# Kernel optimization log

Hardware: AMD Instinct MI355X
Metric: run time of the kernel (lower is better)

Reference implementation:

```python
import jax, jax.numpy as jnp
import numpy as np
import math

C = 256
NUM_CLASSES = 80
NUM_CONVS = 4
GROUPS = 32
LEVEL_SHAPES = [(100, 152), (50, 76), (25, 38), (13, 19), (7, 10)]
BATCH = 2


def conv2d(x, w, b):
    # x: [N,C,H,W], w: [O,I,3,3] -> SAME padding, stride 1
    y = jax.lax.conv_general_dilated(x, w, window_strides=(1, 1), padding='SAME',
                                     dimension_numbers=('NCHW', 'OIHW', 'NCHW'))
    return y + b[None, :, None, None]


def group_norm(x, w, b, groups=GROUPS, eps=1e-5):
    N, Ch, H, W = x.shape
    xg = x.reshape(N, groups, Ch // groups, H, W)
    mu = jnp.mean(xg, axis=(2, 3, 4), keepdims=True)
    var = jnp.var(xg, axis=(2, 3, 4), keepdims=True)
    xg = (xg - mu) * jax.lax.rsqrt(var + eps)
    x = xg.reshape(N, Ch, H, W)
    return x * w[None, :, None, None] + b[None, :, None, None]


def tower(x, cw, cb, gw, gb):
    for i in range(NUM_CONVS):
        x = jax.nn.relu(group_norm(conv2d(x, cw[i], cb[i]), gw[i], gb[i]))
    return x


def flatten_head(y, c):
    # [N, A*c, H, W] -> [N, H*W*A, c]  (matches view/permute/reshape in torch)
    N, AC, H, W = y.shape
    A = AC // c
    return y.reshape(N, A, c, H, W).transpose(0, 3, 4, 1, 2).reshape(N, H * W * A, c)


def setup_inputs() -> dict:
    key = jax.random.key(0)
    ks = iter(jax.random.split(key, 64))
    inp = {}
    for i, (h, w) in enumerate(LEVEL_SHAPES):
        inp[f"feat{i}"] = jax.random.normal(next(ks), (BATCH, C, h, w), jnp.float32)
    def cw(shape):  # conv weights init std=0.01 as in torch module
        return jax.random.normal(next(ks), shape, jnp.float32) * 0.01
    inp["cls_conv_w"] = cw((NUM_CONVS, C, C, 3, 3))
    inp["cls_conv_b"] = jnp.zeros((NUM_CONVS, C), jnp.float32)
    inp["cls_gn_w"] = jnp.ones((NUM_CONVS, C), jnp.float32)
    inp["cls_gn_b"] = jnp.zeros((NUM_CONVS, C), jnp.float32)
    inp["cls_out_w"] = cw((NUM_CLASSES, C, 3, 3))
    inp["cls_out_b"] = jnp.full((NUM_CLASSES,), -math.log(99.0), jnp.float32)  # prior prob 0.01
    inp["reg_conv_w"] = cw((NUM_CONVS, C, C, 3, 3))
    inp["reg_conv_b"] = jnp.zeros((NUM_CONVS, C), jnp.float32)
    inp["reg_gn_w"] = jnp.ones((NUM_CONVS, C), jnp.float32)
    inp["reg_gn_b"] = jnp.zeros((NUM_CONVS, C), jnp.float32)
    for name, oc in [("bbox", 4), ("ctr", 1), ("dim", 3), ("ori", 1), ("kp", 16), ("depth", 1)]:
        inp[f"{name}_w"] = cw((oc, C, 3, 3))
        inp[f"{name}_b"] = jnp.zeros((oc,), jnp.float32)
    return inp


def reference(feat0, feat1, feat2, feat3, feat4,
              cls_conv_w, cls_conv_b, cls_gn_w, cls_gn_b, cls_out_w, cls_out_b,
              reg_conv_w, reg_conv_b, reg_gn_w, reg_gn_b,
              bbox_w, bbox_b, ctr_w, ctr_b, dim_w, dim_b,
              ori_w, ori_b, kp_w, kp_b, depth_w, depth_b):
    feats = [feat0, feat1, feat2, feat3, feat4]
    cls_all, bbox_all, ctr_all, dim_all, ori_all, kp_all, depth_all = ([] for _ in range(7))
    for f in feats:
        cf = tower(f, cls_conv_w, cls_conv_b, cls_gn_w, cls_gn_b)
        cls_all.append(flatten_head(conv2d(cf, cls_out_w, cls_out_b), NUM_CLASSES))
        rf = tower(f, reg_conv_w, reg_conv_b, reg_gn_w, reg_gn_b)
        bbox_all.append(flatten_head(jax.nn.relu(conv2d(rf, bbox_w, bbox_b)), 4))
        ctr_all.append(flatten_head(conv2d(rf, ctr_w, ctr_b), 1))
        dim_all.append(flatten_head(conv2d(rf, dim_w, dim_b), 3))
        ori_all.append(flatten_head(conv2d(rf, ori_w, ori_b), 1))
        kp_all.append(flatten_head(conv2d(rf, kp_w, kp_b), 16))
        depth_all.append(flatten_head(conv2d(rf, depth_w, depth_b), 1))
    cat = lambda xs: jnp.concatenate(xs, axis=1)
    return (cat(cls_all), cat(bbox_all), cat(ctr_all), cat(dim_all),
            cat(ori_all), cat(kp_all), cat(depth_all))
```

## Files before the change

### kernel.cpp

```cpp
#include <hip/hip_runtime.h>
#include <stdint.h>

typedef unsigned short ushort_t;
typedef __bf16 bf16x8 __attribute__((ext_vector_type(8)));
typedef float f32x4 __attribute__((ext_vector_type(4)));

#define TOTAL_HW 20267
#define PTOT 21267

__constant__ int d_RB[26] = {3242720,3242720,3242720,3242720, 3404856, 3445390,3445390,3445390,
                             3566992, 3607526,3607526,3607526,3607526,3607526,3607526,3607526,3607526,
                             3607526,3607526,3607526,3607526,3607526,3607526,3607526,3607526, 4256070};
__constant__ int d_RM[26] = {4,4,4,4, 1, 3,3,3, 1, 16,16,16,16,16,16,16,16,16,16,16,16,16,16,16,16, 1};
__constant__ int d_RC[26] = {0,1,2,3, 0, 0,1,2, 0, 0,1,2,3,4,5,6,7,8,9,10,11,12,13,14,15, 0};

__constant__ int F_TC[6]   = {0,238,298,314,318,320};
__constant__ int F_TL[5]   = {119,30,8,2,1};
__constant__ int F_W[5]    = {152,76,38,19,10};
__constant__ int F_HW[5]   = {15200,3800,950,247,70};
__constant__ int F_PB[5]   = {0,15708,19764,20844,21159};
__constant__ int F_LOFF[5] = {0,15200,19000,19950,20197};
__constant__ int F_PC[6]   = {0,508,764,894,962,1000};
__constant__ int F_H[5]    = {100,50,25,13,7};

__device__ __forceinline__ ushort_t f2bf(float f) {
    union { float f; uint32_t i; } x; x.f = f;
    uint32_t r = x.i + 0x7fffu + ((x.i >> 16) & 1u);
    return (ushort_t)(r >> 16);
}
__device__ __forceinline__ float bf2f(ushort_t u) {
    union { uint32_t i; float f; } x; x.i = ((uint32_t)u) << 16; return x.f;
}
__device__ __forceinline__ void gld16(const ushort_t* g, ushort_t* lds) {
    __builtin_amdgcn_global_load_lds((const __attribute__((address_space(1))) void*)g,
                                     (__attribute__((address_space(3))) void*)lds, 16, 0, 0);
}

__global__ __launch_bounds__(256) void wtrans_tower_k(const float* __restrict__ src,
                                                      ushort_t* __restrict__ dst)
{
    int id = blockIdx.x * 256 + threadIdx.x;
    int oc = id >> 8, ic = id & 255;
    const float* s = src + (size_t)(oc * 256 + ic) * 9;
    ushort_t* d = dst + oc * 256 + ic;
    #pragma unroll
    for (int t = 0; t < 9; t++) d[t * 65536] = f2bf(s[t]);
}
__global__ __launch_bounds__(256) void wtrans_cls_k(const float* __restrict__ src,
                                                    ushort_t* __restrict__ dst)
{
    int id = blockIdx.x * 256 + threadIdx.x;
    int oc = id >> 8, ic = id & 255;
    ushort_t* d = dst + oc * 256 + ic;
    if (oc < 80) {
        const float* s = src + (size_t)(oc * 256 + ic) * 9;
        #pragma unroll
        for (int t = 0; t < 9; t++) d[t * 32768] = f2bf(s[t]);
    } else {
        #pragma unroll
        for (int t = 0; t < 9; t++) d[t * 32768] = 0;
    }
}
__global__ __launch_bounds__(256) void wtrans_reg_k(
    const float* bbox_w, const float* ctr_w, const float* dim_w,
    const float* ori_w,  const float* kp_w,  const float* depth_w,
    const float* bbox_b, const float* ctr_b, const float* dim_b,
    const float* ori_b,  const float* kp_b,  const float* depth_b,
    ushort_t* __restrict__ dst, float* __restrict__ RegBias)
{
    int id = blockIdx.x * 256 + threadIdx.x;
    int oc = id >> 8, ic = id & 255;
    ushort_t* d = dst + oc * 256 + ic;
    if (oc < 26) {
        const float* s; int c;
        if (oc < 4)       { s = bbox_w;  c = oc; }
        else if (oc < 5)  { s = ctr_w;   c = 0; }
        else if (oc < 8)  { s = dim_w;   c = oc - 5; }
        else if (oc < 9)  { s = ori_w;   c = 0; }
        else if (oc < 25) { s = kp_w;    c = oc - 9; }
        else              { s = depth_w; c = 0; }
        const float* sp = s + (size_t)(c * 256 + ic) * 9;
        #pragma unroll
        for (int t = 0; t < 9; t++) d[t * 32768] = f2bf(sp[t]);
    } else {
        #pragma unroll
        for (int t = 0; t < 9; t++) d[t * 32768] = 0;
    }
    if (id < 26) {
        const float* b; int c;
        if (id < 4)       { b = bbox_b;  c = id; }
        else if (id < 5)  { b = ctr_b;   c = 0; }
        else if (id < 8)  { b = dim_b;   c = id - 5; }
        else if (id < 9)  { b = ori_b;   c = 0; }
        else if (id < 25) { b = kp_b;    c = id - 9; }
        else              { b = depth_b; c = 0; }
        RegBias[id] = b[c];
    }
}

__global__ __launch_bounds__(256) void pad_k(ushort_t* b0, ushort_t* b1, ushort_t* b2, ushort_t* b3)
{
    int u = blockIdx.x * 256 + threadIdx.x;
    if (u >= 256000) return;
    int chunk = u & 31; u >>= 5;
    int buf = u & 3; u >>= 2;
    int n = (u >= 1000) ? 1 : 0; int pidx = u - n * 1000;
    int l = 0;
    #pragma unroll
    for (int i = 1; i < 5; i++) if (pidx >= F_PC[i]) l = i;
    int q = pidx - F_PC[l];
    int W = F_W[l], H = F_H[l], Wp = W + 2;
    int py, px;
    if (q < Wp) { py = 0; px = q; }
    else if (q < 2 * Wp) { py = H + 1; px = q - Wp; }
    else { int q2 = q - 2 * Wp; py = 1 + (q2 >> 1); px = (q2 & 1) ? (Wp - 1) : 0; }
    ushort_t* base = b0;
    if (buf == 1) base = b1; else if (buf == 2) base = b2; else if (buf == 3) base = b3;
    *(uint4*)(base + ((size_t)n * PTOT + F_PB[l] + py * Wp + px) * 256 + chunk * 8) = uint4{0u,0u,0u,0u};
}

__global__ __launch_bounds__(256) void packF_k(
    const float* f0, const float* f1, const float* f2,
    const float* f3, const float* f4, ushort_t* __restrict__ S)
{
    __shared__ ushort_t tile[64][65];
    const int PCUM[6] = {0, 1904, 2384, 2504, 2536, 2552};
    const int PT[5]   = {238, 60, 15, 4, 2};
    int bid = blockIdx.x;
    int l = 0;
    #pragma unroll
    for (int i = 1; i < 5; i++) if (bid >= PCUM[i]) l = i;
    int r = bid - PCUM[l];
    int per_n = PT[l] * 4;
    int n = (r >= per_n) ? 1 : 0; r -= n * per_n;
    int pb = r >> 2, cb = r & 3;
    const float* fs = f0;
    if (l == 1) fs = f1; else if (l == 2) fs = f2; else if (l == 3) fs = f3; else if (l == 4) fs = f4;
    int HW = F_HW[l], W = F_W[l], Wp = W + 2;
    int p0 = pb * 64, c0 = cb * 64;
    int t = threadIdx.x;
    #pragma unroll
    for (int i = 0; i < 16; i++) {
        int idx = i * 256 + t; int cl = idx >> 6, pl = idx & 63;
        int p = p0 + pl; ushort_t v = 0;
        if (p < HW) v = f2bf(fs[(size_t)(n * 256 + c0 + cl) * HW + p]);
        tile[cl][pl] = v;
    }
    __syncthreads();
    ushort_t* ob = S + ((size_t)n * PTOT + F_PB[l]) * 256;
    #pragma unroll
    for (int i = 0; i < 16; i++) {
        int idx = i * 256 + t; int pl = idx >> 6, cl = idx & 63;
        int p = p0 + pl;
        if (p < HW) {
            int y = p / W, x = p - y * W;
            ob[((y + 1) * Wp + (x + 1)) * 256 + c0 + cl] = tile[cl][pl];
        }
    }
}

__global__ __launch_bounds__(256) void convT_k(
    const ushort_t* __restrict__ srcC, const ushort_t* __restrict__ srcR,
    ushort_t* __restrict__ dstC, ushort_t* __restrict__ dstR,
    const ushort_t* __restrict__ wtAll,
    const float* __restrict__ biasC, const float* __restrict__ biasR,
    float* __restrict__ stats, int L)
{
    __shared__ __align__(16) ushort_t As[2][4096];
    __shared__ __align__(16) ushort_t Bs[2][4096];

    int gid = blockIdx.x;
    int xcd = gid & 7, idx = gid >> 3;
    int bid = xcd * 40 + (idx >> 2);
    int oc0 = (idx & 1) * 128;
    int tw = (idx >> 1) & 1;

    const ushort_t* src = tw ? srcR : srcC;
    ushort_t* dst = tw ? dstR : dstC;
    const ushort_t* wt = wtAll + (size_t)(tw * 4 + L) * 589824;
    const float* bias = (tw ? biasR : biasC) + L * 256;

    int l = 0;
    #pragma unroll
    for (int i = 1; i < 5; i++) if (bid >= F_TC[i]) l = i;
    int r = bid - F_TC[l];
    int tl = F_TL[l];
    int n = (r >= tl) ? 1 : 0; int tile = r - n * tl;
    int W = F_W[l], HW = F_HW[l], Wp = W + 2;
    int px0 = tile * 128;
    const ushort_t* sbase = src + ((size_t)n * PTOT + F_PB[l]) * 256;
    ushort_t* obase = dst + ((size_t)n * PTOT + F_PB[l]) * 256;

    int tid = threadIdx.x, wv = tid >> 6, ln = tid & 63;
    int wr = wv >> 1, wc = wv & 1;

    int aoff[2], boff[2];
    #pragma unroll
    for (int j = 0; j < 2; j++) {
        int rloc = (wv * 2 + j) * 16 + (ln >> 2);
        int p = px0 + rloc; if (p > HW - 1) p = HW - 1;
        int y = p / W, x = p - y * W;
        int c = ((ln & 3) - (rloc >> 1)) & 3;
        aoff[j] = ((y + 1) * Wp + (x + 1)) * 256 + c * 8;
        boff[j] = (oc0 + rloc) * 256 + c * 8;
    }

    f32x4 acc[4][4];
    #pragma unroll
    for (int mi = 0; mi < 4; mi++)
        #pragma unroll
        for (int ni = 0; ni < 4; ni++) acc[mi][ni] = f32x4{0.f, 0.f, 0.f, 0.f};

    {
        int tapo = (-Wp - 1) * 256;
        #pragma unroll
        for (int j = 0; j < 2; j++) gld16(sbase + aoff[j] + tapo, &As[0][(wv * 2 + j) * 512]);
        #pragma unroll
        for (int j = 0; j < 2; j++) gld16(wt + boff[j], &Bs[0][(wv * 2 + j) * 512]);
    }

    #pragma unroll 2
    for (int it = 0; it < 72; ++it) {
        __syncthreads();
        int nx = it + 1;
        if (nx < 72) {
            int tp = nx >> 3, kc = (nx & 7) << 5;
            int ky = tp / 3, kx = tp - ky * 3;
            int tapo = ((ky - 1) * Wp + (kx - 1)) * 256 + kc;
            const ushort_t* wtap = wt + tp * 65536 + kc;
            int b = nx & 1;
            #pragma unroll
            for (int j = 0; j < 2; j++) gld16(sbase + aoff[j] + tapo, &As[b][(wv * 2 + j) * 512]);
            #pragma unroll
            for (int j = 0; j < 2; j++) gld16(wtap + boff[j], &Bs[b][(wv * 2 + j) * 512]);
        }
        int b = it & 1;
        bf16x8 af[4], bg[4];
        #pragma unroll
        for (int mi = 0; mi < 4; mi++) {
            int rA = wr * 64 + mi * 16 + (ln & 15);
            int ch = ((ln >> 4) + (rA >> 1)) & 3;
            af[mi] = *(const bf16x8*)&As[b][rA * 32 + ch * 8];
        }
        #pragma unroll
        for (int ni = 0; ni < 4; ni++) {
            int rB = wc * 64 + ni * 16 + (ln & 15);
            int ch = ((ln >> 4) + (rB >> 1)) & 3;
            bg[ni] = *(const bf16x8*)&Bs[b][rB * 32 + ch * 8];
        }
        #pragma unroll
        for (int mi = 0; mi < 4; mi++)
            #pragma unroll
            for (int ni = 0; ni < 4; ni++)
                acc[mi][ni] = __builtin_amdgcn_mfma_f32_16x16x32_bf16(af[mi], bg[ni], acc[mi][ni], 0, 0, 0);
    }

    #pragma unroll
    for (int ni = 0; ni < 4; ni++) {
        int oc = oc0 + wc * 64 + ni * 16 + (ln & 15);
        float bv = bias[oc];
        float s = 0.f, q = 0.f;
        #pragma unroll
        for (int mi = 0; mi < 4; mi++) {
            int pb = px0 + wr * 64 + mi * 16 + ((ln >> 4) << 2);
            if (pb < HW) {
                int y = pb / W, x = pb - y * W;
                #pragma unroll
                for (int rr2 = 0; rr2 < 4; rr2++) {
                    int p = pb + rr2;
                    if (p < HW) {
                        float v = acc[mi][ni][rr2] + bv;
                        obase[((y + 1) * Wp + (x + 1)) * 256 + oc] = f2bf(v);
                        s += v; q += v * v;
                    }
                    x++; if (x == W) { x = 0; y++; }
                }
            }
        }
        s += __shfl_xor(s, 16, 64); q += __shfl_xor(q, 16, 64);
        s += __shfl_xor(s, 32, 64); q += __shfl_xor(q, 32, 64);
        s += __shfl_xor(s, 1, 64);  q += __shfl_xor(q, 1, 64);
        s += __shfl_xor(s, 2, 64);  q += __shfl_xor(q, 2, 64);
        s += __shfl_xor(s, 4, 64);  q += __shfl_xor(q, 4, 64);
        if (ln == 0 || ln == 8) {
            int g = (oc0 + wc * 64 + ni * 16 + (ln & 8)) >> 3;
            float* st = stats + (size_t)((tw * 4 + L) * 5 + l) * 128 + (n * 32 + g) * 2;
            atomicAdd(st, s); atomicAdd(st + 1, q);
        }
    }
}

__global__ __launch_bounds__(256) void convH_k(
    const ushort_t* __restrict__ srcC, const ushort_t* __restrict__ srcR,
    const ushort_t* __restrict__ wtC, const ushort_t* __restrict__ wtR,
    const float* __restrict__ biasC, const float* __restrict__ biasR,
    float* __restrict__ outF)
{
    __shared__ __align__(16) ushort_t As[2][4096];
    __shared__ __align__(16) ushort_t Bs[2][4096];

    int gid = blockIdx.x;
    int xcd = gid & 7, idx = gid >> 3;
    int bid = xcd * 40 + (idx >> 1);
    int mode = idx & 1;

    const ushort_t* src = mode ? srcR : srcC;
    const ushort_t* wt  = mode ? wtR  : wtC;
    const float* bias   = mode ? biasR : biasC;

    int l = 0;
    #pragma unroll
    for (int i = 1; i < 5; i++) if (bid >= F_TC[i]) l = i;
    int r = bid - F_TC[l];
    int tl = F_TL[l];
    int n = (r >= tl) ? 1 : 0; int tile = r - n * tl;
    int W = F_W[l], HW = F_HW[l], Wp = W + 2;
    int px0 = tile * 128;
    const ushort_t* sbase = src + ((size_t)n * PTOT + F_PB[l]) * 256;

    int tid = threadIdx.x, wv = tid >> 6, ln = tid & 63;
    int wr = wv >> 1, wc = wv & 1;

    int aoff[2], boff[2];
    #pragma unroll
    for (int j = 0; j < 2; j++) {
        int rloc = (wv * 2 + j) * 16 + (ln >> 2);
        int p = px0 + rloc; if (p > HW - 1) p = HW - 1;
        int y = p / W, x = p - y * W;
        int c = ((ln & 3) - (rloc >> 1)) & 3;
        aoff[j] = ((y + 1) * Wp + (x + 1)) * 256 + c * 8;
        boff[j] = rloc * 256 + c * 8;
    }

    f32x4 acc[4][4];
    #pragma unroll
    for (int mi = 0; mi < 4; mi++)
        #pragma unroll
        for (int ni = 0; ni < 4; ni++) acc[mi][ni] = f32x4{0.f, 0.f, 0.f, 0.f};

    {
        int tapo = (-Wp - 1) * 256;
        #pragma unroll
        for (int j = 0; j < 2; j++) gld16(sbase + aoff[j] + tapo, &As[0][(wv * 2 + j) * 512]);
        #pragma unroll
        for (int j = 0; j < 2; j++) gld16(wt + boff[j], &Bs[0][(wv * 2 + j) * 512]);
    }

    #pragma unroll 2
    for (int it = 0; it < 72; ++it) {
        __syncthreads();
        int nx = it + 1;
        if (nx < 72) {
            int tp = nx >> 3, kc = (nx & 7) << 5;
            int ky = tp / 3, kx = tp - ky * 3;
            int tapo = ((ky - 1) * Wp + (kx - 1)) * 256 + kc;
            const ushort_t* wtap = wt + tp * 32768 + kc;
            int b = nx & 1;
            #pragma unroll
            for (int j = 0; j < 2; j++) gld16(sbase + aoff[j] + tapo, &As[b][(wv * 2 + j) * 512]);
            #pragma unroll
            for (int j = 0; j < 2; j++) gld16(wtap + boff[j], &Bs[b][(wv * 2 + j) * 512]);
        }
        int b = it & 1;
        bf16x8 af[4], bg[4];
        #pragma unroll
        for (int mi = 0; mi < 4; mi++) {
            int rA = wr * 64 + mi * 16 + (ln & 15);
            int ch = ((ln >> 4) + (rA >> 1)) & 3;
            af[mi] = *(const bf16x8*)&As[b][rA * 32 + ch * 8];
        }
        #pragma unroll
        for (int ni = 0; ni < 4; ni++) {
            int rB = wc * 64 + ni * 16 + (ln & 15);
            int ch = ((ln >> 4) + (rB >> 1)) & 3;
            bg[ni] = *(const bf16x8*)&Bs[b][rB * 32 + ch * 8];
        }
        #pragma unroll
        for (int mi = 0; mi < 4; mi++)
            #pragma unroll
            for (int ni = 0; ni < 4; ni++)
                acc[mi][ni] = __builtin_amdgcn_mfma_f32_16x16x32_bf16(af[mi], bg[ni], acc[mi][ni], 0, 0, 0);
    }

    #pragma unroll
    for (int ni = 0; ni < 4; ni++) {
        int oc = wc * 64 + ni * 16 + (ln & 15);
        bool valid = mode ? (oc < 26) : (oc < 80);
        if (valid) {
            float bv = bias[oc];
            int rb = 0, rm = 80, rc = oc; bool rl = false;
            if (mode) { rb = d_RB[oc]; rm = d_RM[oc]; rc = d_RC[oc]; rl = (oc < 4); }
            #pragma unroll
            for (int mi = 0; mi < 4; mi++) {
                int pb = px0 + wr * 64 + mi * 16 + ((ln >> 4) << 2);
                #pragma unroll
                for (int rr2 = 0; rr2 < 4; rr2++) {
                    int p = pb + rr2;
                    if (p < HW) {
                        float v = acc[mi][ni][rr2] + bv;
                        if (rl) v = fmaxf(v, 0.f);
                        int pg = n * TOTAL_HW + F_LOFF[l] + p;
                        outF[rb + (size_t)pg * rm + rc] = v;
                    }
                }
            }
        }
    }
}

__global__ __launch_bounds__(256) void normF_k(
    ushort_t* __restrict__ bufC, ushort_t* __restrict__ bufR,
    const float* __restrict__ stats,
    const float* __restrict__ gwC, const float* __restrict__ gwR,
    const float* __restrict__ gbC, const float* __restrict__ gbR, int L)
{
    int u = blockIdx.x * 256 + threadIdx.x;
    if (u >= 2594176) return;
    int tw = (u >= 1297088) ? 1 : 0; u -= tw * 1297088;
    int n = (u >= 648544) ? 1 : 0; u -= n * 648544;
    int cp = u >> 5, g = u & 31;
    int l = 0;
    #pragma unroll
    for (int i = 1; i < 5; i++) if (cp >= F_LOFF[i]) l = i;
    int p = cp - F_LOFF[l];
    int W = F_W[l], HW = F_HW[l];
    int y = p / W, x = p - y * W;
    const float* st = stats + (size_t)((tw * 4 + L) * 5 + l) * 128 + (n * 32 + g) * 2;
    float cnt = 8.0f * (float)HW;
    float mean = st[0] / cnt;
    float var = st[1] / cnt - mean * mean;
    float inv = rsqrtf(fmaxf(var, 0.f) + 1e-5f);
    const float* gw = (tw ? gwR : gwC) + L * 256 + g * 8;
    const float* gb = (tw ? gbR : gbC) + L * 256 + g * 8;
    ushort_t* buf = tw ? bufR : bufC;
    ushort_t* ptr = buf + (((size_t)n * PTOT + F_PB[l]) + (y + 1) * (W + 2) + (x + 1)) * 256 + g * 8;
    uint4 din = *(const uint4*)ptr;
    uint4 dout;
    const ushort_t* xi = (const ushort_t*)&din;
    ushort_t* oi = (ushort_t*)&dout;
    #pragma unroll
    for (int i = 0; i < 8; i++) {
        float v = (bf2f(xi[i]) - mean) * inv * gw[i] + gb[i];
        oi[i] = f2bf(fmaxf(v, 0.f));
    }
    *(uint4*)ptr = dout;
}


extern "C" void kernel_launch(void* const* d_in, const int* in_sizes, int n_in,
                              void* d_out, int out_size, void* d_ws, size_t ws_size,
                              hipStream_t stream) {
    const float* feats[5] = {(const float*)d_in[0], (const float*)d_in[1],
                             (const float*)d_in[2], (const float*)d_in[3],
                             (const float*)d_in[4]};
    const float* cls_conv_w = (const float*)d_in[5];
    const float* cls_conv_b = (const float*)d_in[6];
    const float* cls_gn_w   = (const float*)d_in[7];
    const float* cls_gn_b   = (const float*)d_in[8];
    const float* cls_out_w  = (const float*)d_in[9];
    const float* cls_out_b  = (const float*)d_in[10];
    const float* reg_conv_w = (const float*)d_in[11];
    const float* reg_conv_b = (const float*)d_in[12];
    const float* reg_gn_w   = (const float*)d_in[13];
    const float* reg_gn_b   = (const float*)d_in[14];

    char* wsb = (char*)d_ws;
    float* Stats     = (float*)wsb;
    float* RegBias   = (float*)(wsb + 20480);
    ushort_t* TowerWtAll = (ushort_t*)(wsb + 20608);
    ushort_t* WtCls  = (ushort_t*)(wsb + 9457792);
    ushort_t* WtReg  = (ushort_t*)(wsb + 10047616);
    ushort_t* S  = (ushort_t*)(wsb + 10637440);
    ushort_t* Ac = (ushort_t*)(wsb + 32414848);
    ushort_t* Ar = (ushort_t*)(wsb + 54192256);
    ushort_t* Br = (ushort_t*)(wsb + 75969664);
    float* outf  = (float*)d_out;

    hipMemsetAsync(d_ws, 0, 20608, stream);
    pad_k<<<1000, 256, 0, stream>>>(S, Ac, Ar, Br);

    for (int tw = 0; tw < 2; tw++) {
        const float* conv_w = tw ? reg_conv_w : cls_conv_w;
        for (int L = 0; L < 4; L++)
            wtrans_tower_k<<<256, 256, 0, stream>>>(conv_w + (size_t)L * 589824,
                                                    TowerWtAll + (size_t)(tw * 4 + L) * 589824);
    }
    wtrans_cls_k<<<128, 256, 0, stream>>>(cls_out_w, WtCls);
    wtrans_reg_k<<<128, 256, 0, stream>>>(
        (const float*)d_in[15], (const float*)d_in[17], (const float*)d_in[19],
        (const float*)d_in[21], (const float*)d_in[23], (const float*)d_in[25],
        (const float*)d_in[16], (const float*)d_in[18], (const float*)d_in[20],
        (const float*)d_in[22], (const float*)d_in[24], (const float*)d_in[26],
        WtReg, RegBias);

    packF_k<<<2552, 256, 0, stream>>>(feats[0], feats[1], feats[2], feats[3], feats[4], S);

    ushort_t* sc[4] = {S,  Ac, S,  Ac};
    ushort_t* dc[4] = {Ac, S,  Ac, S };
    ushort_t* sr[4] = {S,  Ar, Br, Ar};
    ushort_t* dr[4] = {Ar, Br, Ar, Br};
    for (int L = 0; L < 4; L++) {
        convT_k<<<1280, 256, 0, stream>>>(
            sc[L], sr[L], dc[L], dr[L], TowerWtAll, cls_conv_b, reg_conv_b, Stats, L);
        normF_k<<<10134, 256, 0, stream>>>(
            dc[L], dr[L], Stats, cls_gn_w, reg_gn_w, cls_gn_b, reg_gn_b, L);
    }
    convH_k<<<640, 256, 0, stream>>>(S, Br, WtCls, WtReg, cls_out_b, RegBias, outf);
}
```

Baseline: 919.4 us.

## Triple-buffer conv GEMM LDS tiles with partial vmcnt waits and MFMA priority

Moves the convT and convH implicit-GEMM main loops from double to triple LDS buffering, prefetching two K-steps ahead. The full __syncthreads is replaced by an inline s_waitcnt vmcnt(4) plus s_barrier, so only the older in-flight global-to-LDS loads must complete before each step. MFMA blocks are wrapped in s_setprio to favour matrix issue. LDS use per block grows from 32KB to 48KB, which may reduce occupancy, and the hand-written vmcnt counting depends on each step issuing exactly four loads per thread.

```diff
diff --git a/kernel.cpp b/kernel.cpp
--- a/kernel.cpp
+++ b/kernel.cpp
@@ -166,8 +166,8 @@
     const float* __restrict__ biasC, const float* __restrict__ biasR,
     float* __restrict__ stats, int L)
 {
-    __shared__ __align__(16) ushort_t As[2][4096];
-    __shared__ __align__(16) ushort_t Bs[2][4096];
+    __shared__ __align__(16) ushort_t As[3][4096];
+    __shared__ __align__(16) ushort_t Bs[3][4096];
 
     int gid = blockIdx.x;
     int xcd = gid & 7, idx = gid >> 3;
@@ -217,24 +217,33 @@
         for (int j = 0; j < 2; j++) gld16(sbase + aoff[j] + tapo, &As[0][(wv * 2 + j) * 512]);
         #pragma unroll
         for (int j = 0; j < 2; j++) gld16(wt + boff[j], &Bs[0][(wv * 2 + j) * 512]);
-    }
-
-    #pragma unroll 2
+        asm volatile("" ::: "memory");
+        #pragma unroll
+        for (int j = 0; j < 2; j++) gld16(sbase + aoff[j] + tapo + 32, &As[1][(wv * 2 + j) * 512]);
+        #pragma unroll
+        for (int j = 0; j < 2; j++) gld16(wt + 32 + boff[j], &Bs[1][(wv * 2 + j) * 512]);
+    }
+
+    #pragma unroll 3
     for (int it = 0; it < 72; ++it) {
-        __syncthreads();
-        int nx = it + 1;
+        if (it < 71) {
+            asm volatile("s_waitcnt vmcnt(4) lgkmcnt(0)\n\ts_barrier" ::: "memory");
+        } else {
+            asm volatile("s_waitcnt vmcnt(0) lgkmcnt(0)\n\ts_barrier" ::: "memory");
+        }
+        int nx = it + 2;
         if (nx < 72) {
             int tp = nx >> 3, kc = (nx & 7) << 5;
             int ky = tp / 3, kx = tp - ky * 3;
             int tapo = ((ky - 1) * Wp + (kx - 1)) * 256 + kc;
             const ushort_t* wtap = wt + tp * 65536 + kc;
-            int b = nx & 1;
-            #pragma unroll
-            for (int j = 0; j < 2; j++) gld16(sbase + aoff[j] + tapo, &As[b][(wv * 2 + j) * 512]);
-            #pragma unroll
-            for (int j = 0; j < 2; j++) gld16(wtap + boff[j], &Bs[b][(wv * 2 + j) * 512]);
-        }
-        int b = it & 1;
+            int bs = nx % 3;
+            #pragma unroll
+            for (int j = 0; j < 2; j++) gld16(sbase + aoff[j] + tapo, &As[bs][(wv * 2 + j) * 512]);
+            #pragma unroll
+            for (int j = 0; j < 2; j++) gld16(wtap + boff[j], &Bs[bs][(wv * 2 + j) * 512]);
+        }
+        int b = it % 3;
         bf16x8 af[4], bg[4];
         #pragma unroll
         for (int mi = 0; mi < 4; mi++) {
@@ -248,11 +257,13 @@
             int ch = ((ln >> 4) + (rB >> 1)) & 3;
             bg[ni] = *(const bf16x8*)&Bs[b][rB * 32 + ch * 8];
         }
+        __builtin_amdgcn_s_setprio(1);
         #pragma unroll
         for (int mi = 0; mi < 4; mi++)
             #pragma unroll
             for (int ni = 0; ni < 4; ni++)
                 acc[mi][ni] = __builtin_amdgcn_mfma_f32_16x16x32_bf16(af[mi], bg[ni], acc[mi][ni], 0, 0, 0);
+        __builtin_amdgcn_s_setprio(0);
     }
 
     #pragma unroll
@@ -296,8 +307,8 @@
     const float* __restrict__ biasC, const float* __restrict__ biasR,
     float* __restrict__ outF)
 {
-    __shared__ __align__(16) ushort_t As[2][4096];
-    __shared__ __align__(16) ushort_t Bs[2][4096];
+    __shared__ __align__(16) ushort_t As[3][4096];
+    __shared__ __align__(16) ushort_t Bs[3][4096];
 
     int gid = blockIdx.x;
     int xcd = gid & 7, idx = gid >> 3;
@@ -344,24 +355,33 @@
         for (int j = 0; j < 2; j++) gld16(sbase + aoff[j] + tapo, &As[0][(wv * 2 + j) * 512]);
         #pragma unroll
         for (int j = 0; j < 2; j++) gld16(wt + boff[j], &Bs[0][(wv * 2 + j) * 512]);
-    }
-
-    #pragma unroll 2
+        asm volatile("" ::: "memory");
+        #pragma unroll
+        for (int j = 0; j < 2; j++) gld16(sbase + aoff[j] + tapo + 32, &As[1][(wv * 2 + j) * 512]);
+        #pragma unroll
+        for (int j = 0; j < 2; j++) gld16(wt + 32 + boff[j], &Bs[1][(wv * 2 + j) * 512]);
+    }
+
+    #pragma unroll 3
     for (int it = 0; it < 72; ++it) {
-        __syncthreads();
-        int nx = it + 1;
+        if (it < 71) {
+            asm volatile("s_waitcnt vmcnt(4) lgkmcnt(0)\n\ts_barrier" ::: "memory");
+        } else {
+            asm volatile("s_waitcnt vmcnt(0) lgkmcnt(0)\n\ts_barrier" ::: "memory");
+        }
+        int nx = it + 2;
         if (nx < 72) {
             int tp = nx >> 3, kc = (nx & 7) << 5;
             int ky = tp / 3, kx = tp - ky * 3;
             int tapo = ((ky - 1) * Wp + (kx - 1)) * 256 + kc;
             const ushort_t* wtap = wt + tp * 32768 + kc;
-            int b = nx & 1;
-            #pragma unroll
-            for (int j = 0; j < 2; j++) gld16(sbase + aoff[j] + tapo, &As[b][(wv * 2 + j) * 512]);
-            #pragma unroll
-            for (int j = 0; j < 2; j++) gld16(wtap + boff[j], &Bs[b][(wv * 2 + j) * 512]);
-        }
-        int b = it & 1;
+            int bs = nx % 3;
+            #pragma unroll
+            for (int j = 0; j < 2; j++) gld16(sbase + aoff[j] + tapo, &As[bs][(wv * 2 + j) * 512]);
+            #pragma unroll
+            for (int j = 0; j < 2; j++) gld16(wtap + boff[j], &Bs[bs][(wv * 2 + j) * 512]);
+        }
+        int b = it % 3;
         bf16x8 af[4], bg[4];
         #pragma unroll
         for (int mi = 0; mi < 4; mi++) {
@@ -375,11 +395,13 @@
             int ch = ((ln >> 4) + (rB >> 1)) & 3;
             bg[ni] = *(const bf16x8*)&Bs[b][rB * 32 + ch * 8];
         }
+        __builtin_amdgcn_s_setprio(1);
         #pragma unroll
         for (int mi = 0; mi < 4; mi++)
             #pragma unroll
             for (int ni = 0; ni < 4; ni++)
                 acc[mi][ni] = __builtin_amdgcn_mfma_f32_16x16x32_bf16(af[mi], bg[ni], acc[mi][ni], 0, 0, 0);
+        __builtin_amdgcn_s_setprio(0);
     }
 
     #pragma unroll
```

New measurement: 911.0 us. About the same (-0.9%).
